# Kernel optimization log

Measured on AMD Instinct MI355X. Metric: run time of the kernel, lower is better.

The kernel has to match this reference:

```python
import jax, jax.numpy as jnp
import numpy as np

BLOCKS, LAYERS, KS = 4, 2, 2
DILATIONS = [2 ** i for _ in range(BLOCKS) for i in range(LAYERS)]  # [1,2]*4
B, C_IN, N, T = 16, 2, 2048, 12
RC, DC, SC, EC, OUT = 32, 32, 256, 512, 12
L = BLOCKS * LAYERS
BN_EPS = 1e-5


def setup_inputs() -> dict:
    key = jax.random.key(0)
    ks = jax.random.split(key, 24)
    # raw inputs
    x = jax.random.normal(ks[0], (B, C_IN, N, T), dtype=jnp.float32)
    # two fixed supports: row-normalized random adjacency (dense, as in GraphWaveNet transition matrices)
    A_raw = jax.random.uniform(ks[1], (2, N, N), dtype=jnp.float32)
    A = A_raw / jnp.sum(A_raw, axis=2, keepdims=True)
    nodevec1 = jax.random.normal(ks[2], (N, 10), dtype=jnp.float32)
    nodevec2 = jax.random.normal(ks[3], (10, N), dtype=jnp.float32)
    s = 0.1  # weight scale to keep activations in a sane range
    filter_w = jax.random.normal(ks[4], (L, DC, RC, KS), dtype=jnp.float32) * s
    filter_b = jax.random.normal(ks[5], (L, DC), dtype=jnp.float32) * s
    gate_w = jax.random.normal(ks[6], (L, DC, RC, KS), dtype=jnp.float32) * s
    gate_b = jax.random.normal(ks[7], (L, DC), dtype=jnp.float32) * s
    skip_w = jax.random.normal(ks[8], (L, SC, DC), dtype=jnp.float32) * s
    skip_b = jax.random.normal(ks[9], (L, SC), dtype=jnp.float32) * s
    gcn_w = jax.random.normal(ks[10], (L, RC, 7 * DC), dtype=jnp.float32) * s
    gcn_b = jax.random.normal(ks[11], (L, RC), dtype=jnp.float32) * s
    bn_gamma = 1.0 + 0.1 * jax.random.normal(ks[12], (L, RC), dtype=jnp.float32)
    bn_beta = 0.1 * jax.random.normal(ks[13], (L, RC), dtype=jnp.float32)
    bn_mean = 0.1 * jax.random.normal(ks[14], (L, RC), dtype=jnp.float32)
    bn_var = 1.0 + jax.random.uniform(ks[15], (L, RC), dtype=jnp.float32)
    start_w = jax.random.normal(ks[16], (RC, C_IN), dtype=jnp.float32) * s
    start_b = jax.random.normal(ks[17], (RC,), dtype=jnp.float32) * s
    end1_w = jax.random.normal(ks[18], (EC, SC), dtype=jnp.float32) * s
    end1_b = jax.random.normal(ks[19], (EC,), dtype=jnp.float32) * s
    end2_w = jax.random.normal(ks[20], (OUT, EC), dtype=jnp.float32) * s
    end2_b = jax.random.normal(ks[21], (OUT,), dtype=jnp.float32) * s
    return dict(x=x, A=A, nodevec1=nodevec1, nodevec2=nodevec2,
                filter_w=filter_w, filter_b=filter_b, gate_w=gate_w, gate_b=gate_b,
                skip_w=skip_w, skip_b=skip_b, gcn_w=gcn_w, gcn_b=gcn_b,
                bn_gamma=bn_gamma, bn_beta=bn_beta, bn_mean=bn_mean, bn_var=bn_var,
                start_w=start_w, start_b=start_b, end1_w=end1_w, end1_b=end1_b,
                end2_w=end2_w, end2_b=end2_b)


def _conv1x1(x, w, b):
    # x: [b,c,n,t], w: [o,c] -> [b,o,n,t]
    return jnp.einsum('oc,bcnt->bont', w, x) + b[None, :, None, None]


def _dilated_conv2(x, w, b, d):
    # kernel (1,2) with time dilation d; out length T-d (valid conv)
    xa, xb = x[..., :-d], x[..., d:]
    y = jnp.einsum('oc,bcnt->bont', w[:, :, 0], xa) + jnp.einsum('oc,bcnt->bont', w[:, :, 1], xb)
    return y + b[None, :, None, None]


def _fwd(x, A, nodevec1, nodevec2, filter_w, filter_b, gate_w, gate_b,
         skip_w, skip_b, gcn_w, gcn_b, bn_gamma, bn_beta, bn_mean, bn_var,
         start_w, start_b, end1_w, end1_b, end2_w, end2_b):
    # pad 1 step at the start of time; T becomes 13 == receptive_field
    x = jnp.pad(x, ((0, 0), (0, 0), (0, 0), (1, 0)))
    x = x[:, :2]
    x = _conv1x1(x, start_w, start_b)  # [B,RC,N,13]
    # adaptive adjacency
    adp = jax.nn.softmax(jax.nn.relu(nodevec1 @ nodevec2), axis=1)
    supports = [A[0], A[1], adp]
    skip = None
    for i, d in enumerate(DILATIONS):
        residual = x
        filt = jnp.tanh(_dilated_conv2(residual, filter_w[i], filter_b[i], d))
        gate = jax.nn.sigmoid(_dilated_conv2(residual, gate_w[i], gate_b[i], d))
        x = filt * gate  # [B,DC,N,T-d]
        s = _conv1x1(x, skip_w[i], skip_b[i])  # [B,SC,N,T']
        skip = s if skip is None else s + skip[..., -s.shape[3]:]
        # GCN: order-2 diffusion over 3 supports, concat, 1x1 mix (dropout is identity in eval)
        outs = [x]
        for a in supports:
            x1 = jnp.einsum('bcvt,vw->bcwt', x, a)
            x2 = jnp.einsum('bcvt,vw->bcwt', x1, a)
            outs.extend([x1, x2])
        h = jnp.concatenate(outs, axis=1)  # [B,7*DC,N,T']
        x = _conv1x1(h, gcn_w[i], gcn_b[i])
        x = x + residual[..., -x.shape[3]:]
        # BatchNorm2d in eval mode (running stats)
        inv = bn_gamma[i] / jnp.sqrt(bn_var[i] + BN_EPS)
        x = (x - bn_mean[i][None, :, None, None]) * inv[None, :, None, None] + bn_beta[i][None, :, None, None]
    x = jax.nn.relu(skip)
    x = jax.nn.relu(_conv1x1(x, end1_w, end1_b))
    x = _conv1x1(x, end2_w, end2_b)  # [B,OUT,N,1]
    return x


def reference(x, A, nodevec1, nodevec2, filter_w, filter_b, gate_w, gate_b,
              skip_w, skip_b, gcn_w, gcn_b, bn_gamma, bn_beta, bn_mean, bn_var,
              start_w, start_b, end1_w, end1_b, end2_w, end2_b):
    return _fwd(x, A, nodevec1, nodevec2, filter_w, filter_b, gate_w, gate_b,
                skip_w, skip_b, gcn_w, gcn_b, bn_gamma, bn_beta, bn_mean, bn_var,
                start_w, start_b, end1_w, end1_b, end2_w, end2_b)
```

## Files before the change

kernel.cpp:

```cpp
#include <hip/hip_runtime.h>
#include <math.h>


#define NNODE 2048
#define NLAYER 8
#define SSTR ((size_t)NNODE * NNODE)

typedef unsigned short u16;
typedef unsigned int u32;
typedef __attribute__((ext_vector_type(8))) short bf16x8;
typedef __attribute__((ext_vector_type(4))) float f32x4;

__device__ __forceinline__ u16 f2bf(float f) {
    unsigned u = __builtin_bit_cast(unsigned, f);
    u += 0x7fffu + ((u >> 16) & 1u);
    return (u16)(u >> 16);
}
__device__ __forceinline__ float bf2f(u16 h) {
    unsigned u = ((unsigned)h) << 16;
    return __builtin_bit_cast(float, u);
}
__device__ __forceinline__ float bflo(u32 p) { return __builtin_bit_cast(float, p << 16); }
__device__ __forceinline__ float bfhi(u32 p) { return __builtin_bit_cast(float, p & 0xffff0000u); }
__device__ __forceinline__ u32 pack2(float a, float b) {
    return (u32)f2bf(a) | ((u32)f2bf(b) << 16);
}

__device__ __forceinline__ void gld16(const void* g, void* l) {
    __builtin_amdgcn_global_load_lds(
        (const __attribute__((address_space(1))) unsigned int*)g,
        (__attribute__((address_space(3))) unsigned int*)l, 16, 0, 0);
}

__global__ __launch_bounds__(256) void k_adp_mm(const float* __restrict__ nv1,
                                                const float* __restrict__ nv2,
                                                float* __restrict__ P) {
    int v = blockIdx.y;
    int w = blockIdx.x * 256 + threadIdx.x;
    float acc = 0.f;
#pragma unroll
    for (int k = 0; k < 10; ++k) acc += nv1[v * 10 + k] * nv2[k * NNODE + w];
    P[(size_t)v * NNODE + w] = acc;
}

__global__ __launch_bounds__(256) void k_softmax(float* __restrict__ P) {
    int v = blockIdx.x, tid = threadIdx.x;
    float* row = P + (size_t)v * NNODE;
    float m = 0.f;
    for (int w = tid; w < NNODE; w += 256) m = fmaxf(m, fmaxf(row[w], 0.f));
#pragma unroll
    for (int off = 32; off > 0; off >>= 1) m = fmaxf(m, __shfl_down(m, off));
    __shared__ float redm[4];
    __shared__ float reds[4];
    int wave = tid >> 6, lane = tid & 63;
    if (lane == 0) redm[wave] = m;
    __syncthreads();
    m = fmaxf(fmaxf(redm[0], redm[1]), fmaxf(redm[2], redm[3]));
    float s = 0.f;
    for (int w = tid; w < NNODE; w += 256) s += expf(fmaxf(row[w], 0.f) - m);
#pragma unroll
    for (int off = 32; off > 0; off >>= 1) s += __shfl_down(s, off);
    if (lane == 0) reds[wave] = s;
    __syncthreads();
    s = reds[0] + reds[1] + reds[2] + reds[3];
    float inv = 1.f / s;
    for (int w = tid; w < NNODE; w += 256) row[w] = expf(fmaxf(row[w], 0.f) - m) * inv;
}

__global__ __launch_bounds__(256) void k_transp(const float* __restrict__ A,
                                                const float* __restrict__ adp,
                                                u16* __restrict__ ST,
                                                u16* __restrict__ Sbf) {
    __shared__ float tile[32][33];
    int s = blockIdx.z;
    const float* src = (s < 2) ? (A + (size_t)s * SSTR) : adp;
    int v0 = blockIdx.y * 32, w0 = blockIdx.x * 32;
    int tx = threadIdx.x & 31, ty = threadIdx.x >> 5;
    u16* dst2 = Sbf + (size_t)s * SSTR;
#pragma unroll
    for (int p = 0; p < 4; ++p) {
        float v = src[(size_t)(v0 + ty + p * 8) * NNODE + w0 + tx];
        tile[ty + p * 8][tx] = v;
        dst2[(size_t)(v0 + ty + p * 8) * NNODE + w0 + tx] = f2bf(v);
    }
    __syncthreads();
    u16* dst = ST + (size_t)(2 * s) * SSTR;
#pragma unroll
    for (int p = 0; p < 4; ++p)
        dst[(size_t)(w0 + ty + p * 8) * NNODE + v0 + tx] = f2bf(tile[tx][ty + p * 8]);
}

__global__ __launch_bounds__(256) void k_skprep(const float* __restrict__ skw,
                                                const float* __restrict__ skb,
                                                u16* __restrict__ skwB,
                                                float* __restrict__ skbsum) {
    int idx = blockIdx.x * 256 + threadIdx.x;
    int sc = idx >> 8, k = idx & 255, l = k >> 5, ci = k & 31;
    skwB[idx] = f2bf(skw[((size_t)l * 256 + sc) * 32 + ci]);
    if (blockIdx.x == 0) {
        float s = 0.f;
#pragma unroll
        for (int ll = 0; ll < 8; ++ll) s += skb[ll * 256 + threadIdx.x];
        skbsum[threadIdx.x] = s;
    }
}

__global__ __launch_bounds__(512, 2) void k_gemmS(const u16* __restrict__ ST,
                                                  const u16* __restrict__ Sbf) {
    __shared__ __align__(16) char ldsb[131072];
    const int tid = threadIdx.x;
    const int wave = tid >> 6, lane = tid & 63;
    const int m0 = blockIdx.y * 256;
    const int slice = blockIdx.x >> 3;
    const int n0 = (blockIdx.x & 7) * 256;
    const u16* AbG = ST + (size_t)(2 * slice) * SSTR + (size_t)m0 * 2048;
    const u16* BbG = Sbf + (size_t)slice * SSTR + (size_t)n0 * 2048;

    const int xorc = ((tid & 7) ^ ((tid >> 3) & 7)) << 3;
    const size_t aRow = (size_t)(tid >> 3) * 2048 + xorc;
    const int bRowLoc = ((tid >> 8) << 6) + (((tid >> 6) & 3) << 3) + ((tid >> 3) & 7);
    const size_t bRow = (size_t)bRowLoc * 2048 + xorc;
    const int aw = wave << 10;
    const int bw = ((wave >> 2) << 13) + ((wave & 3) << 10);

    const int fr = lane & 15;
    const int cl4 = lane >> 4;
    const int ch0 = (cl4 ^ (fr & 7)) << 4;
    const int ch1 = ch0 ^ 64;
    const int aRd = ((wave & 1) << 14) + fr * 128;
    const int bRd = ((wave >> 1) << 13) + fr * 128;
    const int wm = (wave & 1) << 7;
    const int wn = (wave >> 1) << 6;

    char* A0 = ldsb;
    char* A1 = ldsb + 32768;
    char* B0 = ldsb + 65536;
    char* B1 = ldsb + 98304;

    auto STA = [&](char* Abase, int k0, int q) {
        const size_t g = (size_t)(q << 6) * 2048 + aRow + k0;
        gld16(AbG + g, Abase + (q << 13) + aw);
        gld16(AbG + g + (size_t)128 * 2048, Abase + 16384 + (q << 13) + aw);
    };
    auto STB = [&](char* Bbase, int k0, int q) {
        const size_t g = (size_t)(q << 5) * 2048 + bRow + k0;
        gld16(BbG + g, Bbase + (q << 12) + bw);
        gld16(BbG + g + (size_t)128 * 2048, Bbase + 16384 + (q << 12) + bw);
    };

    f32x4 acc[8][4];
#pragma unroll
    for (int i = 0; i < 8; ++i)
#pragma unroll
        for (int j = 0; j < 4; ++j) acc[i][j] = (f32x4){0.f, 0.f, 0.f, 0.f};

    STA(A0, 0, 0); STA(A0, 0, 1); STB(B0, 0, 0); STB(B0, 0, 1);
    STA(A1, 64, 0); STB(B1, 64, 0); STB(B1, 64, 1);
    asm volatile("s_waitcnt vmcnt(6)" ::: "memory");
    asm volatile("s_barrier" ::: "memory");

    char *Ac = A0, *Ao = A1, *Bc = B0, *Bo = B1;
    bf16x8 af[4][2], bfl[2][2], bfh[2][2];

    for (int T = 0; T < 32; ++T) {
#pragma unroll
        for (int i = 0; i < 4; ++i) {
            af[i][0] = *(const bf16x8*)(Ac + aRd + (i << 11) + ch0);
            af[i][1] = *(const bf16x8*)(Ac + aRd + (i << 11) + ch1);
        }
#pragma unroll
        for (int j = 0; j < 2; ++j) {
            bfl[j][0] = *(const bf16x8*)(Bc + bRd + (j << 11) + ch0);
            bfl[j][1] = *(const bf16x8*)(Bc + bRd + (j << 11) + ch1);
        }
        if (T < 31) STA(Ao, (T + 1) * 64, 1);
        asm volatile("s_barrier" ::: "memory");
        asm volatile("s_waitcnt lgkmcnt(0)" ::: "memory");
        __builtin_amdgcn_sched_barrier(0);
        __builtin_amdgcn_s_setprio(1);
#pragma unroll
        for (int i = 0; i < 4; ++i)
#pragma unroll
            for (int j = 0; j < 2; ++j) {
                acc[i][j] = __builtin_amdgcn_mfma_f32_16x16x32_bf16(af[i][0], bfl[j][0], acc[i][j], 0, 0, 0);
                acc[i][j] = __builtin_amdgcn_mfma_f32_16x16x32_bf16(af[i][1], bfl[j][1], acc[i][j], 0, 0, 0);
            }
        __builtin_amdgcn_s_setprio(0);
#pragma unroll
        for (int j = 0; j < 2; ++j) {
            bfh[j][0] = *(const bf16x8*)(Bc + bRd + 4096 + (j << 11) + ch0);
            bfh[j][1] = *(const bf16x8*)(Bc + bRd + 4096 + (j << 11) + ch1);
        }
        asm volatile("s_barrier" ::: "memory");
        asm volatile("s_waitcnt lgkmcnt(0)" ::: "memory");
        __builtin_amdgcn_sched_barrier(0);
        __builtin_amdgcn_s_setprio(1);
#pragma unroll
        for (int i = 0; i < 4; ++i)
#pragma unroll
            for (int j = 0; j < 2; ++j) {
                acc[i][2 + j] = __builtin_amdgcn_mfma_f32_16x16x32_bf16(af[i][0], bfh[j][0], acc[i][2 + j], 0, 0, 0);
                acc[i][2 + j] = __builtin_amdgcn_mfma_f32_16x16x32_bf16(af[i][1], bfh[j][1], acc[i][2 + j], 0, 0, 0);
            }
        __builtin_amdgcn_s_setprio(0);
#pragma unroll
        for (int i = 0; i < 4; ++i) {
            af[i][0] = *(const bf16x8*)(Ac + aRd + 8192 + (i << 11) + ch0);
            af[i][1] = *(const bf16x8*)(Ac + aRd + 8192 + (i << 11) + ch1);
        }
        if (T < 30) { STA(Ac, (T + 2) * 64, 0); STB(Bc, (T + 2) * 64, 0); }
        asm volatile("s_barrier" ::: "memory");
        asm volatile("s_waitcnt lgkmcnt(0)" ::: "memory");
        __builtin_amdgcn_sched_barrier(0);
        __builtin_amdgcn_s_setprio(1);
#pragma unroll
        for (int i = 0; i < 4; ++i)
#pragma unroll
            for (int j = 0; j < 2; ++j) {
                acc[4 + i][2 + j] = __builtin_amdgcn_mfma_f32_16x16x32_bf16(af[i][0], bfh[j][0], acc[4 + i][2 + j], 0, 0, 0);
                acc[4 + i][2 + j] = __builtin_amdgcn_mfma_f32_16x16x32_bf16(af[i][1], bfh[j][1], acc[4 + i][2 + j], 0, 0, 0);
            }
        __builtin_amdgcn_s_setprio(0);
        if (T < 30) STB(Bc, (T + 2) * 64, 1);
        asm volatile("s_barrier" ::: "memory");
        __builtin_amdgcn_sched_barrier(0);
        __builtin_amdgcn_s_setprio(1);
#pragma unroll
        for (int i = 0; i < 4; ++i)
#pragma unroll
            for (int j = 0; j < 2; ++j) {
                acc[4 + i][j] = __builtin_amdgcn_mfma_f32_16x16x32_bf16(af[i][0], bfl[j][0], acc[4 + i][j], 0, 0, 0);
                acc[4 + i][j] = __builtin_amdgcn_mfma_f32_16x16x32_bf16(af[i][1], bfl[j][1], acc[4 + i][j], 0, 0, 0);
            }
        __builtin_amdgcn_s_setprio(0);
        if (T < 30) {
            asm volatile("s_waitcnt vmcnt(6)" ::: "memory");
        } else if (T == 30) {
            asm volatile("s_waitcnt vmcnt(0)" ::: "memory");
        }
        asm volatile("s_barrier" ::: "memory");
        char* t;
        t = Ac; Ac = Ao; Ao = t;
        t = Bc; Bc = Bo; Bo = t;
    }

    u16* Cb = (u16*)ST + (size_t)(2 * slice + 1) * SSTR + (size_t)(m0 + wm) * 2048 + n0 + wn;
    const int orow = cl4 * 4;
#pragma unroll
    for (int i = 0; i < 8; ++i)
#pragma unroll
        for (int j = 0; j < 4; ++j)
#pragma unroll
            for (int r = 0; r < 4; ++r)
                Cb[(size_t)(i * 16 + orow + r) * 2048 + j * 16 + fr] = f2bf(acc[i][j][r]);
}

__global__ __launch_bounds__(512, 2) void k_gemmZ(const u16* __restrict__ Xg,
                                                  const u16* __restrict__ ST,
                                                  u16* __restrict__ Z, int pass) {
    __shared__ __align__(16) char ldsb[131072];
    const int tid = threadIdx.x;
    const int wave = tid >> 6, lane = tid & 63;
    const int m0 = blockIdx.y * 256;
    const int slice = pass * 3 + (blockIdx.x >> 3);
    const int n0 = (blockIdx.x & 7) * 256;
    const u16* AbG = Xg + (size_t)m0 * 2048;
    const u16* BbG = ST + (size_t)slice * SSTR + (size_t)n0 * 2048;

    const int xorc = ((tid & 7) ^ ((tid >> 3) & 7)) << 3;
    const size_t aRow = (size_t)(tid >> 3) * 2048 + xorc;
    const int bRowLoc = ((tid >> 8) << 6) + (((tid >> 6) & 3) << 3) + ((tid >> 3) & 7);
    const size_t bRow = (size_t)bRowLoc * 2048 + xorc;
    const int aw = wave << 10;
    const int bw = ((wave >> 2) << 13) + ((wave & 3) << 10);

    const int fr = lane & 15;
    const int cl4 = lane >> 4;
    const int ch0 = (cl4 ^ (fr & 7)) << 4;
    const int ch1 = ch0 ^ 64;
    const int aRd = ((wave & 1) << 14) + fr * 128;
    const int bRd = ((wave >> 1) << 13) + fr * 128;
    const int wm = (wave & 1) << 7;
    const int wn = (wave >> 1) << 6;

    char* A0 = ldsb;
    char* A1 = ldsb + 32768;
    char* B0 = ldsb + 65536;
    char* B1 = ldsb + 98304;

    auto STA = [&](char* Abase, int k0, int q) {
        const size_t g = (size_t)(q << 6) * 2048 + aRow + k0;
        gld16(AbG + g, Abase + (q << 13) + aw);
        gld16(AbG + g + (size_t)128 * 2048, Abase + 16384 + (q << 13) + aw);
    };
    auto STB = [&](char* Bbase, int k0, int q) {
        const size_t g = (size_t)(q << 5) * 2048 + bRow + k0;
        gld16(BbG + g, Bbase + (q << 12) + bw);
        gld16(BbG + g + (size_t)128 * 2048, Bbase + 16384 + (q << 12) + bw);
    };

    f32x4 acc[8][4];
#pragma unroll
    for (int i = 0; i < 8; ++i)
#pragma unroll
        for (int j = 0; j < 4; ++j) acc[i][j] = (f32x4){0.f, 0.f, 0.f, 0.f};

    STA(A0, 0, 0); STA(A0, 0, 1); STB(B0, 0, 0); STB(B0, 0, 1);
    STA(A1, 64, 0); STB(B1, 64, 0); STB(B1, 64, 1);
    asm volatile("s_waitcnt vmcnt(6)" ::: "memory");
    asm volatile("s_barrier" ::: "memory");

    char *Ac = A0, *Ao = A1, *Bc = B0, *Bo = B1;
    bf16x8 af[4][2], bfl[2][2], bfh[2][2];

    for (int T = 0; T < 32; ++T) {
#pragma unroll
        for (int i = 0; i < 4; ++i) {
            af[i][0] = *(const bf16x8*)(Ac + aRd + (i << 11) + ch0);
            af[i][1] = *(const bf16x8*)(Ac + aRd + (i << 11) + ch1);
        }
#pragma unroll
        for (int j = 0; j < 2; ++j) {
            bfl[j][0] = *(const bf16x8*)(Bc + bRd + (j << 11) + ch0);
            bfl[j][1] = *(const bf16x8*)(Bc + bRd + (j << 11) + ch1);
        }
        if (T < 31) STA(Ao, (T + 1) * 64, 1);
        asm volatile("s_barrier" ::: "memory");
        asm volatile("s_waitcnt lgkmcnt(0)" ::: "memory");
        __builtin_amdgcn_sched_barrier(0);
        __builtin_amdgcn_s_setprio(1);
#pragma unroll
        for (int i = 0; i < 4; ++i)
#pragma unroll
            for (int j = 0; j < 2; ++j) {
                acc[i][j] = __builtin_amdgcn_mfma_f32_16x16x32_bf16(af[i][0], bfl[j][0], acc[i][j], 0, 0, 0);
                acc[i][j] = __builtin_amdgcn_mfma_f32_16x16x32_bf16(af[i][1], bfl[j][1], acc[i][j], 0, 0, 0);
            }
        __builtin_amdgcn_s_setprio(0);
#pragma unroll
        for (int j = 0; j < 2; ++j) {
            bfh[j][0] = *(const bf16x8*)(Bc + bRd + 4096 + (j << 11) + ch0);
            bfh[j][1] = *(const bf16x8*)(Bc + bRd + 4096 + (j << 11) + ch1);
        }
        asm volatile("s_barrier" ::: "memory");
        asm volatile("s_waitcnt lgkmcnt(0)" ::: "memory");
        __builtin_amdgcn_sched_barrier(0);
        __builtin_amdgcn_s_setprio(1);
#pragma unroll
        for (int i = 0; i < 4; ++i)
#pragma unroll
            for (int j = 0; j < 2; ++j) {
                acc[i][2 + j] = __builtin_amdgcn_mfma_f32_16x16x32_bf16(af[i][0], bfh[j][0], acc[i][2 + j], 0, 0, 0);
                acc[i][2 + j] = __builtin_amdgcn_mfma_f32_16x16x32_bf16(af[i][1], bfh[j][1], acc[i][2 + j], 0, 0, 0);
            }
        __builtin_amdgcn_s_setprio(0);
#pragma unroll
        for (int i = 0; i < 4; ++i) {
            af[i][0] = *(const bf16x8*)(Ac + aRd + 8192 + (i << 11) + ch0);
            af[i][1] = *(const bf16x8*)(Ac + aRd + 8192 + (i << 11) + ch1);
        }
        if (T < 30) { STA(Ac, (T + 2) * 64, 0); STB(Bc, (T + 2) * 64, 0); }
        asm volatile("s_barrier" ::: "memory");
        asm volatile("s_waitcnt lgkmcnt(0)" ::: "memory");
        __builtin_amdgcn_sched_barrier(0);
        __builtin_amdgcn_s_setprio(1);
#pragma unroll
        for (int i = 0; i < 4; ++i)
#pragma unroll
            for (int j = 0; j < 2; ++j) {
                acc[4 + i][2 + j] = __builtin_amdgcn_mfma_f32_16x16x32_bf16(af[i][0], bfh[j][0], acc[4 + i][2 + j], 0, 0, 0);
                acc[4 + i][2 + j] = __builtin_amdgcn_mfma_f32_16x16x32_bf16(af[i][1], bfh[j][1], acc[4 + i][2 + j], 0, 0, 0);
            }
        __builtin_amdgcn_s_setprio(0);
        if (T < 30) STB(Bc, (T + 2) * 64, 1);
        asm volatile("s_barrier" ::: "memory");
        __builtin_amdgcn_sched_barrier(0);
        __builtin_amdgcn_s_setprio(1);
#pragma unroll
        for (int i = 0; i < 4; ++i)
#pragma unroll
            for (int j = 0; j < 2; ++j) {
                acc[4 + i][j] = __builtin_amdgcn_mfma_f32_16x16x32_bf16(af[i][0], bfl[j][0], acc[4 + i][j], 0, 0, 0);
                acc[4 + i][j] = __builtin_amdgcn_mfma_f32_16x16x32_bf16(af[i][1], bfl[j][1], acc[4 + i][j], 0, 0, 0);
            }
        __builtin_amdgcn_s_setprio(0);
        if (T < 30) {
            asm volatile("s_waitcnt vmcnt(6)" ::: "memory");
        } else if (T == 30) {
            asm volatile("s_waitcnt vmcnt(0)" ::: "memory");
        }
        asm volatile("s_barrier" ::: "memory");
        char* t;
        t = Ac; Ac = Ao; Ao = t;
        t = Bc; Bc = Bo; Bo = t;
    }

    const int col0 = (blockIdx.x >> 3) * 2048 + (blockIdx.x & 7) * 256;
    u16* Cb = Z + (size_t)(m0 + wm) * 6144 + col0 + wn;
    const int orow = cl4 * 4;
#pragma unroll
    for (int i = 0; i < 8; ++i)
#pragma unroll
        for (int j = 0; j < 4; ++j)
#pragma unroll
            for (int r = 0; r < 4; ++r)
                Cb[(size_t)(i * 16 + orow + r) * 6144 + j * 16 + fr] = f2bf(acc[i][j][r]);
}

__global__ __launch_bounds__(256) void k_gemmZ128(const u16* __restrict__ Xg,
                                                  const u16* __restrict__ ST,
                                                  u16* __restrict__ Z, int pass) {
    __shared__ u16 Asl[2][128 * 32];
    __shared__ u16 Bsl[2][128 * 32];
    const int tid = threadIdx.x;
    const int wave = tid >> 6, lane = tid & 63;
    const int m0 = blockIdx.y * 128;
    const int slice = pass * 3 + (blockIdx.x >> 4);
    const int nIn = (blockIdx.x & 15) * 128;
    const u16* Ab = Xg + (size_t)m0 * 2048;
    const u16* Bb = ST + (size_t)slice * SSTR + (size_t)nIn * NNODE;
    const int tr = tid >> 2;
    const int tc = (tid & 3) * 8;
    char* AslB0 = (char*)Asl[0] + wave * 1024;
    char* AslB1 = (char*)Asl[1] + wave * 1024;
    char* BslB0 = (char*)Bsl[0] + wave * 1024;
    char* BslB1 = (char*)Bsl[1] + wave * 1024;
    const int wm = (wave & 1) * 64, wn = (wave >> 1) * 64;
    const int fr = lane & 15;
    const int fk = (lane >> 4) * 8;
    f32x4 acc[4][4];
#pragma unroll
    for (int i = 0; i < 4; ++i)
#pragma unroll
        for (int j = 0; j < 4; ++j) acc[i][j] = (f32x4){0.f, 0.f, 0.f, 0.f};

    for (int k0 = 0; k0 < 2048; k0 += 64) {
        gld16(Ab + (size_t)tr * 2048 + k0 + tc, AslB0);
        gld16(Ab + (size_t)(tr + 64) * 2048 + k0 + tc, AslB0 + 4096);
        gld16(Ab + (size_t)tr * 2048 + k0 + 32 + tc, AslB1);
        gld16(Ab + (size_t)(tr + 64) * 2048 + k0 + 32 + tc, AslB1 + 4096);
        gld16(Bb + (size_t)tr * NNODE + k0 + tc, BslB0);
        gld16(Bb + (size_t)(tr + 64) * NNODE + k0 + tc, BslB0 + 4096);
        gld16(Bb + (size_t)tr * NNODE + k0 + 32 + tc, BslB1);
        gld16(Bb + (size_t)(tr + 64) * NNODE + k0 + 32 + tc, BslB1 + 4096);
        __syncthreads();
#pragma unroll
        for (int h = 0; h < 2; ++h) {
            bf16x8 af[4], bf[4];
#pragma unroll
            for (int i = 0; i < 4; ++i)
                af[i] = *(const bf16x8*)&Asl[h][(wm + i * 16 + fr) * 32 + fk];
#pragma unroll
            for (int j = 0; j < 4; ++j)
                bf[j] = *(const bf16x8*)&Bsl[h][(wn + j * 16 + fr) * 32 + fk];
#pragma unroll
            for (int i = 0; i < 4; ++i)
#pragma unroll
                for (int j = 0; j < 4; ++j)
                    acc[i][j] = __builtin_amdgcn_mfma_f32_16x16x32_bf16(af[i], bf[j], acc[i][j], 0, 0, 0);
        }
        __syncthreads();
    }
    u16* Cb = Z + (size_t)(m0 + wm) * 6144 + blockIdx.x * 128 + wn;
    const int orow = (lane >> 4) * 4;
#pragma unroll
    for (int i = 0; i < 4; ++i)
#pragma unroll
        for (int j = 0; j < 4; ++j)
#pragma unroll
            for (int r = 0; r < 4; ++r)
                Cb[(size_t)(i * 16 + orow + r) * 6144 + j * 16 + fr] = f2bf(acc[i][j][r]);
}

__global__ __launch_bounds__(256) void k_start(const float* __restrict__ xin,
                                               const float* __restrict__ sw,
                                               const float* __restrict__ sb,
                                               u16* __restrict__ out, int b0) {
    int n = blockIdx.x * 256 + threadIdx.x;
    int t = blockIdx.y;
    int bl = blockIdx.z;
    int b = b0 + bl;
    float x0 = 0.f, x1 = 0.f;
    if (t > 0) {
        x0 = xin[((size_t)(b * 2 + 0) * NNODE + n) * 12 + (t - 1)];
        x1 = xin[((size_t)(b * 2 + 1) * NNODE + n) * 12 + (t - 1)];
    }
#pragma unroll
    for (int co = 0; co < 32; ++co) {
        float v = sw[co * 2 + 0] * x0 + sw[co * 2 + 1] * x1 + sb[co];
        out[((size_t)(bl * 32 + co) * 13 + t) * NNODE + n] = f2bf(v);
    }
}

__global__ __launch_bounds__(256) void k_gate(const u16* __restrict__ cur,
                                              u16* __restrict__ xg,
                                              u16* __restrict__ nxt,
                                              int T, int Tn, int d,
                                              const float* __restrict__ fw,
                                              const float* __restrict__ fb,
                                              const float* __restrict__ gw,
                                              const float* __restrict__ gb,
                                              const float* __restrict__ gcwl,
                                              const float* __restrict__ gcbl,
                                              u16* __restrict__ xl,
                                              int layer, int donxt) {
    __shared__ float4 wp[1024];
    __shared__ float w0[32][33];
    int tid = threadIdx.x;
#pragma unroll
    for (int u = 0; u < 4; ++u) {
        int idx = tid + u * 256;
        int ci = idx >> 5, co = idx & 31;
        wp[idx] = make_float4(fw[co * 64 + ci * 2], fw[co * 64 + ci * 2 + 1],
                              gw[co * 64 + ci * 2], gw[co * 64 + ci * 2 + 1]);
        w0[ci][co] = gcwl[co * 224 + ci];
    }
    __syncthreads();
    int n = blockIdx.x * 512 + tid * 2;
    int t = blockIdx.y;
    int bl = blockIdx.z;
    float f0[32], f1[32], g0[32], g1[32];
#pragma unroll
    for (int co = 0; co < 32; ++co) { f0[co] = 0.f; f1[co] = 0.f; g0[co] = 0.f; g1[co] = 0.f; }
    for (int ci = 0; ci < 32; ++ci) {
        size_t ba = ((size_t)(bl * 32 + ci) * T + t) * NNODE + n;
        size_t bb = ((size_t)(bl * 32 + ci) * T + t + d) * NNODE + n;
        u32 ua = *(const u32*)&cur[ba];
        u32 ub = *(const u32*)&cur[bb];
        float xa0 = bflo(ua), xa1 = bfhi(ua);
        float xb0 = bflo(ub), xb1 = bfhi(ub);
#pragma unroll
        for (int co = 0; co < 32; ++co) {
            float4 w = wp[ci * 32 + co];
            f0[co] += w.x * xa0 + w.y * xb0;
            f1[co] += w.x * xa1 + w.y * xb1;
            g0[co] += w.z * xa0 + w.w * xb0;
            g1[co] += w.z * xa1 + w.w * xb1;
        }
    }
#pragma unroll
    for (int co = 0; co < 32; ++co) {
        float fbv = fb[co], gbv = gb[co];
        float a0 = tanhf(f0[co] + fbv) * (1.f / (1.f + expf(-(g0[co] + gbv))));
        float a1 = tanhf(f1[co] + fbv) * (1.f / (1.f + expf(-(g1[co] + gbv))));
        f0[co] = a0; f1[co] = a1;
        size_t o = ((size_t)(bl * 32 + co) * Tn + t) * NNODE + n;
        *(u32*)&xg[o] = pack2(a0, a1);
    }
    if (t == Tn - 1) {
        size_t o2 = ((size_t)(bl * 2048 + n)) * 256 + layer * 32;
#pragma unroll
        for (int co = 0; co < 32; ++co) {
            xl[o2 + co] = f2bf(f0[co]);
            xl[o2 + 256 + co] = f2bf(f1[co]);
        }
    }
    if (donxt) {
#pragma unroll
        for (int cop = 0; cop < 32; ++cop) {
            float s0 = gcbl[cop], s1 = s0;
#pragma unroll
            for (int ci = 0; ci < 32; ++ci) {
                float wv = w0[ci][cop];
                s0 += wv * f0[ci];
                s1 += wv * f1[ci];
            }
            size_t o = ((size_t)(bl * 32 + cop) * Tn + t) * NNODE + n;
            *(u32*)&nxt[o] = pack2(s0, s1);
        }
    }
}

__global__ __launch_bounds__(256) void k_accum(const u16* __restrict__ Z,
                                               int cbase,
                                               const float* __restrict__ gcnw,
                                               u16* __restrict__ outp,
                                               const u16* __restrict__ resid,
                                               int Tn, int d, int finalf,
                                               const float* __restrict__ bng,
                                               const float* __restrict__ bnb,
                                               const float* __restrict__ bnm,
                                               const float* __restrict__ bnv) {
    __shared__ float wl[3][32][32];
    int tid = threadIdx.x;
    for (int u = tid; u < 3072; u += 256) {
        int g = u >> 10, ci = (u >> 5) & 31, co = u & 31;
        wl[g][ci][co] = gcnw[co * 224 + cbase + g * 32 + ci];
    }
    __syncthreads();
    int n = blockIdx.x * 512 + tid * 2;
    int t = blockIdx.y, bl = blockIdx.z;
    float a0[32], a1[32];
#pragma unroll
    for (int co = 0; co < 32; ++co) { a0[co] = 0.f; a1[co] = 0.f; }
    for (int ci = 0; ci < 32; ++ci) {
        size_t m = (size_t)(bl * 32 + ci) * Tn + t;
#pragma unroll
        for (int g = 0; g < 3; ++g) {
            u32 zz = *(const u32*)&Z[m * 6144 + g * 2048 + n];
            float v0 = bflo(zz), v1 = bfhi(zz);
#pragma unroll
            for (int cq = 0; cq < 8; ++cq) {
                float4 w = *(const float4*)&wl[g][ci][cq * 4];
                a0[cq * 4 + 0] += w.x * v0; a1[cq * 4 + 0] += w.x * v1;
                a0[cq * 4 + 1] += w.y * v0; a1[cq * 4 + 1] += w.y * v1;
                a0[cq * 4 + 2] += w.z * v0; a1[cq * 4 + 2] += w.z * v1;
                a0[cq * 4 + 3] += w.w * v0; a1[cq * 4 + 3] += w.w * v1;
            }
        }
    }
#pragma unroll
    for (int co = 0; co < 32; ++co) {
        size_t o = ((size_t)(bl * 32 + co) * Tn + t) * NNODE + n;
        u32 oo = *(const u32*)&outp[o];
        float v0 = bflo(oo) + a0[co];
        float v1 = bfhi(oo) + a1[co];
        if (finalf) {
            size_t ro = ((size_t)(bl * 32 + co) * (Tn + d) + t + d) * NNODE + n;
            u32 rr = *(const u32*)&resid[ro];
            v0 += bflo(rr); v1 += bfhi(rr);
            float inv = bng[co] * rsqrtf(bnv[co] + 1e-5f);
            float mu = bnm[co], be = bnb[co];
            v0 = (v0 - mu) * inv + be;
            v1 = (v1 - mu) * inv + be;
        }
        *(u32*)&outp[o] = pack2(v0, v1);
    }
}

__global__ __launch_bounds__(256) void k_accum2(const u16* __restrict__ Z0,
                                                const u16* __restrict__ Z1,
                                                const float* __restrict__ gcnw,
                                                u16* __restrict__ outp,
                                                const u16* __restrict__ resid,
                                                int Tn, int d,
                                                const float* __restrict__ bng,
                                                const float* __restrict__ bnb,
                                                const float* __restrict__ bnm,
                                                const float* __restrict__ bnv) {
    __shared__ float wl[6][32][32];
    int tid = threadIdx.x;
    for (int u = tid; u < 6144; u += 256) {
        int pg = u >> 10, ci = (u >> 5) & 31, co = u & 31;
        int cbase = (pg < 3) ? (32 + pg * 32) : (128 + (pg - 3) * 32);
        wl[pg][ci][co] = gcnw[co * 224 + cbase + ci];
    }
    __syncthreads();
    int n = blockIdx.x * 512 + tid * 2;
    int t = blockIdx.y, bl = blockIdx.z;
    float a0[32], a1[32];
#pragma unroll
    for (int co = 0; co < 32; ++co) { a0[co] = 0.f; a1[co] = 0.f; }
    for (int ci = 0; ci < 32; ++ci) {
        size_t m = (size_t)(bl * 32 + ci) * Tn + t;
#pragma unroll
        for (int pg = 0; pg < 6; ++pg) {
            const u16* Zs = (pg < 3) ? Z0 : Z1;
            int g = (pg < 3) ? pg : pg - 3;
            u32 zz = *(const u32*)&Zs[m * 6144 + g * 2048 + n];
            float v0 = bflo(zz), v1 = bfhi(zz);
#pragma unroll
            for (int cq = 0; cq < 8; ++cq) {
                float4 w = *(const float4*)&wl[pg][ci][cq * 4];
                a0[cq * 4 + 0] += w.x * v0; a1[cq * 4 + 0] += w.x * v1;
                a0[cq * 4 + 1] += w.y * v0; a1[cq * 4 + 1] += w.y * v1;
                a0[cq * 4 + 2] += w.z * v0; a1[cq * 4 + 2] += w.z * v1;
                a0[cq * 4 + 3] += w.w * v0; a1[cq * 4 + 3] += w.w * v1;
            }
        }
    }
#pragma unroll
    for (int co = 0; co < 32; ++co) {
        size_t o = ((size_t)(bl * 32 + co) * Tn + t) * NNODE + n;
        u32 oo = *(const u32*)&outp[o];
        float v0 = bflo(oo) + a0[co];
        float v1 = bfhi(oo) + a1[co];
        size_t ro = ((size_t)(bl * 32 + co) * (Tn + d) + t + d) * NNODE + n;
        u32 rr = *(const u32*)&resid[ro];
        v0 += bflo(rr); v1 += bfhi(rr);
        float inv = bng[co] * rsqrtf(bnv[co] + 1e-5f);
        float mu = bnm[co], be = bnb[co];
        v0 = (v0 - mu) * inv + be;
        v1 = (v1 - mu) * inv + be;
        *(u32*)&outp[o] = pack2(v0, v1);
    }
}

__global__ __launch_bounds__(256) void k_cast(const float* __restrict__ src,
                                              u16* __restrict__ dst) {
    int i = blockIdx.x * 256 + threadIdx.x;
    dst[i] = f2bf(src[i]);
}

__global__ __launch_bounds__(256) void k_skipg(const u16* __restrict__ xl,
                                               const u16* __restrict__ skwB,
                                               const float* __restrict__ skbsum,
                                               u16* __restrict__ skipT) {
    __shared__ u16 Asl[128 * 32];
    __shared__ u16 Bsl[128 * 32];
    const int tid = threadIdx.x;
    const int wave = tid >> 6, lane = tid & 63;
    const int m0 = blockIdx.y * 128;
    const int n0 = blockIdx.x * 128;
    const int tr = tid >> 2;
    const int tc = (tid & 3) * 8;
    char* AslB = (char*)Asl + wave * 1024;
    char* BslB = (char*)Bsl + wave * 1024;
    const int wm = (wave & 1) * 64, wn = (wave >> 1) * 64;
    const int fr = lane & 15;
    const int fk = (lane >> 4) * 8;
    const u16* Ab = xl + (size_t)m0 * 256;
    const u16* Bb = skwB + (size_t)n0 * 256;
    f32x4 acc[4][4];
#pragma unroll
    for (int i = 0; i < 4; ++i)
#pragma unroll
        for (int j = 0; j < 4; ++j) acc[i][j] = (f32x4){0.f, 0.f, 0.f, 0.f};
    for (int k0 = 0; k0 < 256; k0 += 32) {
        gld16(Ab + (size_t)tr * 256 + k0 + tc, AslB);
        gld16(Ab + (size_t)(tr + 64) * 256 + k0 + tc, AslB + 4096);
        gld16(Bb + (size_t)tr * 256 + k0 + tc, BslB);
        gld16(Bb + (size_t)(tr + 64) * 256 + k0 + tc, BslB + 4096);
        __syncthreads();
        bf16x8 af[4], bf[4];
#pragma unroll
        for (int i = 0; i < 4; ++i)
            af[i] = *(const bf16x8*)&Asl[(wm + i * 16 + fr) * 32 + fk];
#pragma unroll
        for (int j = 0; j < 4; ++j)
            bf[j] = *(const bf16x8*)&Bsl[(wn + j * 16 + fr) * 32 + fk];
#pragma unroll
        for (int i = 0; i < 4; ++i)
#pragma unroll
            for (int j = 0; j < 4; ++j)
                acc[i][j] = __builtin_amdgcn_mfma_f32_16x16x32_bf16(af[i], bf[j], acc[i][j], 0, 0, 0);
        __syncthreads();
    }
    const int orow = (lane >> 4) * 4;
#pragma unroll
    for (int i = 0; i < 4; ++i)
#pragma unroll
        for (int r = 0; r < 4; ++r) {
            int m = m0 + wm + i * 16 + orow + r;
            size_t ob = (size_t)m * 256 + n0 + wn;
#pragma unroll
            for (int j = 0; j < 4; ++j) {
                int col = n0 + wn + j * 16 + fr;
                skipT[ob + j * 16 + fr] = f2bf(fmaxf(acc[i][j][r] + skbsum[col], 0.f));
            }
        }
}

__global__ __launch_bounds__(256) void k_end1m(const u16* __restrict__ E1,
                                               const u16* __restrict__ skT,
                                               const float* __restrict__ bias,
                                               u16* __restrict__ h) {
    __shared__ u16 Asl[128 * 32];
    __shared__ u16 Bsl[128 * 32];
    const int tid = threadIdx.x;
    const int wave = tid >> 6, lane = tid & 63;
    const int b = blockIdx.z;
    const int m0 = blockIdx.y * 128;
    const int n0 = blockIdx.x * 128;
    const int tr = tid >> 2;
    const int tc = (tid & 3) * 8;
    char* AslB = (char*)Asl + wave * 1024;
    char* BslB = (char*)Bsl + wave * 1024;
    const int wm = (wave & 1) * 64, wn = (wave >> 1) * 64;
    const int fr = lane & 15;
    const int fk = (lane >> 4) * 8;
    const u16* Ab = E1 + (size_t)m0 * 256;
    const u16* Bb = skT + ((size_t)b * NNODE + n0) * 256;
    f32x4 acc[4][4];
#pragma unroll
    for (int i = 0; i < 4; ++i)
#pragma unroll
        for (int j = 0; j < 4; ++j) acc[i][j] = (f32x4){0.f, 0.f, 0.f, 0.f};
    for (int k0 = 0; k0 < 256; k0 += 32) {
        gld16(Ab + (size_t)tr * 256 + k0 + tc, AslB);
        gld16(Ab + (size_t)(tr + 64) * 256 + k0 + tc, AslB + 4096);
        gld16(Bb + (size_t)tr * 256 + k0 + tc, BslB);
        gld16(Bb + (size_t)(tr + 64) * 256 + k0 + tc, BslB + 4096);
        __syncthreads();
        bf16x8 af[4], bf[4];
#pragma unroll
        for (int i = 0; i < 4; ++i)
            af[i] = *(const bf16x8*)&Asl[(wm + i * 16 + fr) * 32 + fk];
#pragma unroll
        for (int j = 0; j < 4; ++j)
            bf[j] = *(const bf16x8*)&Bsl[(wn + j * 16 + fr) * 32 + fk];
#pragma unroll
        for (int i = 0; i < 4; ++i)
#pragma unroll
            for (int j = 0; j < 4; ++j)
                acc[i][j] = __builtin_amdgcn_mfma_f32_16x16x32_bf16(af[i], bf[j], acc[i][j], 0, 0, 0);
        __syncthreads();
    }
    const int orow = (lane >> 4) * 4;
#pragma unroll
    for (int i = 0; i < 4; ++i)
#pragma unroll
        for (int r = 0; r < 4; ++r) {
            int m = m0 + wm + i * 16 + orow + r;
            float bs = bias[m];
            size_t ob = ((size_t)b * 512 + m) * NNODE + n0 + wn;
#pragma unroll
            for (int j = 0; j < 4; ++j)
                h[ob + j * 16 + fr] = f2bf(fmaxf(acc[i][j][r] + bs, 0.f));
        }
}

__global__ __launch_bounds__(256) void k_end2(const u16* __restrict__ h,
                                              const float* __restrict__ w,
                                              const float* __restrict__ bias,
                                              float* __restrict__ out) {
    __shared__ float wl[12][512];
    int tid = threadIdx.x;
    for (int u = tid; u < 6144; u += 256) wl[u >> 9][u & 511] = w[u];
    __syncthreads();
    int n = blockIdx.x * 256 + tid;
    int b = blockIdx.y;
    float acc[12];
#pragma unroll
    for (int o = 0; o < 12; ++o) acc[o] = 0.f;
#pragma unroll 4
    for (int e = 0; e < 512; ++e) {
        float v = bf2f(h[((size_t)(b * 512) + e) * NNODE + n]);
#pragma unroll
        for (int o = 0; o < 12; ++o) acc[o] += wl[o][e] * v;
    }
#pragma unroll
    for (int o = 0; o < 12; ++o)
        out[((size_t)(b * 12) + o) * NNODE + n] = acc[o] + bias[o];
}

extern "C" void kernel_launch(void* const* d_in, const int* in_sizes, int n_in,
                              void* d_out, int out_size, void* d_ws, size_t ws_size,
                              hipStream_t stream) {
    const float* x_in = (const float*)d_in[0];
    const float* A    = (const float*)d_in[1];
    const float* nv1  = (const float*)d_in[2];
    const float* nv2  = (const float*)d_in[3];
    const float* fw   = (const float*)d_in[4];
    const float* fb   = (const float*)d_in[5];
    const float* gw   = (const float*)d_in[6];
    const float* gb   = (const float*)d_in[7];
    const float* skw  = (const float*)d_in[8];
    const float* skb  = (const float*)d_in[9];
    const float* gcw  = (const float*)d_in[10];
    const float* gcb  = (const float*)d_in[11];
    const float* bng  = (const float*)d_in[12];
    const float* bnb  = (const float*)d_in[13];
    const float* bnm  = (const float*)d_in[14];
    const float* bnv  = (const float*)d_in[15];
    const float* stw  = (const float*)d_in[16];
    const float* stb  = (const float*)d_in[17];
    const float* e1w  = (const float*)d_in[18];
    const float* e1b  = (const float*)d_in[19];
    const float* e2w  = (const float*)d_in[20];
    const float* e2b  = (const float*)d_in[21];
    (void)in_sizes; (void)n_in; (void)out_size;

    const int BL = (ws_size >= 239075328UL) ? 16 : 8;
    const int nch = 16 / BL;
    const size_t bufsz = (size_t)BL * 1703936UL;

    char* base = (char*)d_ws;
    u16*   ST     = (u16*)base;
    u16*   xlast  = (u16*)(base + 50331648UL);
    u16*   skwB   = (u16*)(base + 67108864UL);
    float* skbsum = (float*)(base + 67239936UL);
    u16*   bufA = (u16*)(base + 83886080UL);
    u16*   bufB = (u16*)(base + 83886080UL + bufsz);
    u16*   xg   = (u16*)(base + 83886080UL + 2 * bufsz);
    u16*   Z    = (u16*)(base + 83886080UL + 2 * bufsz + (size_t)BL * 1572864UL);
    float* adp  = (float*)Z;
    u16*   Sbf  = (u16*)bufA;
    u16*   h     = (u16*)(base + 83886080UL);
    u16*   skipT = (u16*)(base + 83886080UL + 33554432UL);
    u16*   E1bf  = (u16*)ST;

    k_adp_mm<<<dim3(8, 2048), 256, 0, stream>>>(nv1, nv2, adp);
    k_skprep<<<256, 256, 0, stream>>>(skw, skb, skwB, skbsum);
    k_softmax<<<2048, 256, 0, stream>>>(adp);
    k_transp<<<dim3(64, 64, 3), 256, 0, stream>>>(A, adp, ST, Sbf);
    k_gemmS<<<dim3(24, 8), 512, 0, stream>>>(ST, Sbf);

    static const int DIL[NLAYER] = {1, 2, 1, 2, 1, 2, 1, 2};
    for (int ch = 0; ch < nch; ++ch) {
        int b0 = ch * BL;
        k_start<<<dim3(8, 13, BL), 256, 0, stream>>>(x_in, stw, stb, bufA, b0);
        u16* cur = bufA;
        u16* nxt = bufB;
        int T = 13;
        for (int i = 0; i < NLAYER; ++i) {
            int d = DIL[i], Tn = T - d;
            int last = (i == NLAYER - 1);
            k_gate<<<dim3(4, Tn, BL), 256, 0, stream>>>(cur, xg, nxt, T, Tn, d,
                fw + i * 2048, fb + i * 32, gw + i * 2048, gb + i * 32,
                gcw + i * 32 * 224, gcb + i * 32,
                xlast + (size_t)b0 * 2048 * 256, i, last ? 0 : 1);
            if (last) break;
            const float* gcwi = gcw + i * 32 * 224;
            const size_t Msz = (size_t)BL * 32 * Tn * 6144;
            const bool canMerge =
                (BL == 16) && (Tn <= 6 || (Tn == 7 && ws_size >= 251658240UL));
            if (Tn == 6 || Tn == 3) {
                if (canMerge) {
                    k_gemmZ128<<<dim3(48, BL * Tn / 4), 256, 0, stream>>>(xg, ST, Z, 0);
                    k_gemmZ128<<<dim3(48, BL * Tn / 4), 256, 0, stream>>>(xg, ST, Z + Msz, 1);
                    k_accum2<<<dim3(4, Tn, BL), 256, 0, stream>>>(
                        Z, Z + Msz, gcwi, nxt, cur, Tn, d,
                        bng + i * 32, bnb + i * 32, bnm + i * 32, bnv + i * 32);
                } else {
                    for (int p = 0; p < 2; ++p) {
                        k_gemmZ128<<<dim3(48, BL * Tn / 4), 256, 0, stream>>>(xg, ST, Z, p);
                        k_accum<<<dim3(4, Tn, BL), 256, 0, stream>>>(
                            Z, 32 + 96 * p, gcwi, nxt, cur, Tn, d, p,
                            bng + i * 32, bnb + i * 32, bnm + i * 32, bnv + i * 32);
                    }
                }
            } else if (canMerge) {
                k_gemmZ<<<dim3(24, BL * 32 * Tn / 256), 512, 0, stream>>>(xg, ST, Z, 0);
                k_gemmZ<<<dim3(24, BL * 32 * Tn / 256), 512, 0, stream>>>(xg, ST, Z + Msz, 1);
                k_accum2<<<dim3(4, Tn, BL), 256, 0, stream>>>(
                    Z, Z + Msz, gcwi, nxt, cur, Tn, d,
                    bng + i * 32, bnb + i * 32, bnm + i * 32, bnv + i * 32);
            } else {
                for (int p = 0; p < 2; ++p) {
                    k_gemmZ<<<dim3(24, BL * 32 * Tn / 256), 512, 0, stream>>>(xg, ST, Z, p);
                    k_accum<<<dim3(4, Tn, BL), 256, 0, stream>>>(
                        Z, 32 + 96 * p, gcwi, nxt, cur, Tn, d, p,
                        bng + i * 32, bnb + i * 32, bnm + i * 32, bnv + i * 32);
                }
            }
            u16* tmp = cur; cur = nxt; nxt = tmp;
            T = Tn;
        }
    }
    k_cast<<<512, 256, 0, stream>>>(e1w, E1bf);
    k_skipg<<<dim3(2, 256), 256, 0, stream>>>(xlast, skwB, skbsum, skipT);
    k_end1m<<<dim3(16, 4, 16), 256, 0, stream>>>(E1bf, skipT, e1b, h);
    k_end2<<<dim3(8, 16), 256, 0, stream>>>(h, e2w, e2b, (float*)d_out);
}
```

Baseline: 2.917 ms.

## Fuse adaptive adjacency matmul with softmax and rebalance the Tn=12 GEMM grid

Merges the nodevec product and the row softmax into one kernel that keeps each row in registers, removing a full write and re-read of the 2048x2048 float matrix. For the Tn=12 layer it replaces two equal GEMM launches with a 32-row-block launch, where the extra blocks compute part of pass 1 into a spare Zx buffer, and a 16-row-block launch for the rest. A new accumulate kernel reads from either buffer depending on the row. It also sends Tn=7 to the 128-tile GEMM path. The aim is better wave quantization across the GPU's compute units, at the cost of more complex buffer bookkeeping and a dependence on a larger workspace.

```diff
diff --git a/kernel.cpp b/kernel.cpp
--- a/kernel.cpp
+++ b/kernel.cpp
@@ -32,22 +32,25 @@
         (__attribute__((address_space(3))) unsigned int*)l, 16, 0, 0);
 }
 
-__global__ __launch_bounds__(256) void k_adp_mm(const float* __restrict__ nv1,
-                                                const float* __restrict__ nv2,
-                                                float* __restrict__ P) {
-    int v = blockIdx.y;
-    int w = blockIdx.x * 256 + threadIdx.x;
-    float acc = 0.f;
-#pragma unroll
-    for (int k = 0; k < 10; ++k) acc += nv1[v * 10 + k] * nv2[k * NNODE + w];
-    P[(size_t)v * NNODE + w] = acc;
-}
-
-__global__ __launch_bounds__(256) void k_softmax(float* __restrict__ P) {
+__global__ __launch_bounds__(256) void k_adpsm(const float* __restrict__ nv1,
+                                               const float* __restrict__ nv2,
+                                               float* __restrict__ P) {
     int v = blockIdx.x, tid = threadIdx.x;
-    float* row = P + (size_t)v * NNODE;
+    float a[10];
+#pragma unroll
+    for (int k = 0; k < 10; ++k) a[k] = nv1[v * 10 + k];
+    float val[8];
     float m = 0.f;
-    for (int w = tid; w < NNODE; w += 256) m = fmaxf(m, fmaxf(row[w], 0.f));
+#pragma unroll
+    for (int u = 0; u < 8; ++u) {
+        int w = tid + u * 256;
+        float acc = 0.f;
+#pragma unroll
+        for (int k = 0; k < 10; ++k) acc += a[k] * nv2[k * NNODE + w];
+        acc = fmaxf(acc, 0.f);
+        val[u] = acc;
+        m = fmaxf(m, acc);
+    }
 #pragma unroll
     for (int off = 32; off > 0; off >>= 1) m = fmaxf(m, __shfl_down(m, off));
     __shared__ float redm[4];
@@ -57,14 +60,17 @@
     __syncthreads();
     m = fmaxf(fmaxf(redm[0], redm[1]), fmaxf(redm[2], redm[3]));
     float s = 0.f;
-    for (int w = tid; w < NNODE; w += 256) s += expf(fmaxf(row[w], 0.f) - m);
+#pragma unroll
+    for (int u = 0; u < 8; ++u) { val[u] = expf(val[u] - m); s += val[u]; }
 #pragma unroll
     for (int off = 32; off > 0; off >>= 1) s += __shfl_down(s, off);
     if (lane == 0) reds[wave] = s;
     __syncthreads();
     s = reds[0] + reds[1] + reds[2] + reds[3];
     float inv = 1.f / s;
-    for (int w = tid; w < NNODE; w += 256) row[w] = expf(fmaxf(row[w], 0.f) - m) * inv;
+#pragma unroll
+    for (int u = 0; u < 8; ++u)
+        P[(size_t)v * NNODE + tid + u * 256] = val[u] * inv;
 }
 
 __global__ __launch_bounds__(256) void k_transp(const float* __restrict__ A,
@@ -257,12 +263,18 @@
 
 __global__ __launch_bounds__(512, 2) void k_gemmZ(const u16* __restrict__ Xg,
                                                   const u16* __restrict__ ST,
-                                                  u16* __restrict__ Z, int pass) {
+                                                  u16* __restrict__ Z, int pass,
+                                                  int mbMain, int mOff,
+                                                  u16* __restrict__ Zx) {
     __shared__ __align__(16) char ldsb[131072];
     const int tid = threadIdx.x;
     const int wave = tid >> 6, lane = tid & 63;
-    const int m0 = blockIdx.y * 256;
-    const int slice = pass * 3 + (blockIdx.x >> 3);
+    int byv = blockIdx.y;
+    int p = pass;
+    u16* Zo = Z;
+    if (byv >= mbMain) { byv -= mbMain; p = 1; Zo = Zx; }
+    const int m0 = (byv + mOff) * 256;
+    const int slice = p * 3 + (blockIdx.x >> 3);
     const int n0 = (blockIdx.x & 7) * 256;
     const u16* AbG = Xg + (size_t)m0 * 2048;
     const u16* BbG = ST + (size_t)slice * SSTR + (size_t)n0 * 2048;
@@ -396,7 +408,7 @@
     }
 
     const int col0 = (blockIdx.x >> 3) * 2048 + (blockIdx.x & 7) * 256;
-    u16* Cb = Z + (size_t)(m0 + wm) * 6144 + col0 + wn;
+    u16* Cb = Zo + (size_t)(m0 + wm) * 6144 + col0 + wn;
     const int orow = cl4 * 4;
 #pragma unroll
     for (int i = 0; i < 8; ++i)
@@ -624,6 +636,63 @@
             v0 = (v0 - mu) * inv + be;
             v1 = (v1 - mu) * inv + be;
         }
+        *(u32*)&outp[o] = pack2(v0, v1);
+    }
+}
+
+__global__ __launch_bounds__(256) void k_accumX(const u16* __restrict__ Z,
+                                                const u16* __restrict__ Zx,
+                                                int splitRow,
+                                                const float* __restrict__ gcnw,
+                                                u16* __restrict__ outp,
+                                                const u16* __restrict__ resid,
+                                                int Tn, int d,
+                                                const float* __restrict__ bng,
+                                                const float* __restrict__ bnb,
+                                                const float* __restrict__ bnm,
+                                                const float* __restrict__ bnv) {
+    __shared__ float wl[3][32][32];
+    int tid = threadIdx.x;
+    for (int u = tid; u < 3072; u += 256) {
+        int g = u >> 10, ci = (u >> 5) & 31, co = u & 31;
+        wl[g][ci][co] = gcnw[co * 224 + 128 + g * 32 + ci];
+    }
+    __syncthreads();
+    int n = blockIdx.x * 512 + tid * 2;
+    int t = blockIdx.y, bl = blockIdx.z;
+    float a0[32], a1[32];
+#pragma unroll
+    for (int co = 0; co < 32; ++co) { a0[co] = 0.f; a1[co] = 0.f; }
+    for (int ci = 0; ci < 32; ++ci) {
+        size_t m = (size_t)(bl * 32 + ci) * Tn + t;
+        const u16* Zs = (m < (size_t)splitRow) ? Zx : Z;
+#pragma unroll
+        for (int g = 0; g < 3; ++g) {
+            u32 zz = *(const u32*)&Zs[m * 6144 + g * 2048 + n];
+            float v0 = bflo(zz), v1 = bfhi(zz);
+#pragma unroll
+            for (int cq = 0; cq < 8; ++cq) {
+                float4 w = *(const float4*)&wl[g][ci][cq * 4];
+                a0[cq * 4 + 0] += w.x * v0; a1[cq * 4 + 0] += w.x * v1;
+                a0[cq * 4 + 1] += w.y * v0; a1[cq * 4 + 1] += w.y * v1;
+                a0[cq * 4 + 2] += w.z * v0; a1[cq * 4 + 2] += w.z * v1;
+                a0[cq * 4 + 3] += w.w * v0; a1[cq * 4 + 3] += w.w * v1;
+            }
+        }
+    }
+#pragma unroll
+    for (int co = 0; co < 32; ++co) {
+        size_t o = ((size_t)(bl * 32 + co) * Tn + t) * NNODE + n;
+        u32 oo = *(const u32*)&outp[o];
+        float v0 = bflo(oo) + a0[co];
+        float v1 = bfhi(oo) + a1[co];
+        size_t ro = ((size_t)(bl * 32 + co) * (Tn + d) + t + d) * NNODE + n;
+        u32 rr = *(const u32*)&resid[ro];
+        v0 += bflo(rr); v1 += bfhi(rr);
+        float inv = bng[co] * rsqrtf(bnv[co] + 1e-5f);
+        float mu = bnm[co], be = bnb[co];
+        v0 = (v0 - mu) * inv + be;
+        v1 = (v1 - mu) * inv + be;
         *(u32*)&outp[o] = pack2(v0, v1);
     }
 }
@@ -874,15 +943,15 @@
     u16*   bufB = (u16*)(base + 83886080UL + bufsz);
     u16*   xg   = (u16*)(base + 83886080UL + 2 * bufsz);
     u16*   Z    = (u16*)(base + 83886080UL + 2 * bufsz + (size_t)BL * 1572864UL);
+    u16*   Zx   = (u16*)(base + 239075328UL);
     float* adp  = (float*)Z;
     u16*   Sbf  = (u16*)bufA;
     u16*   h     = (u16*)(base + 83886080UL);
     u16*   skipT = (u16*)(base + 83886080UL + 33554432UL);
     u16*   E1bf  = (u16*)ST;
 
-    k_adp_mm<<<dim3(8, 2048), 256, 0, stream>>>(nv1, nv2, adp);
+    k_adpsm<<<2048, 256, 0, stream>>>(nv1, nv2, adp);
     k_skprep<<<256, 256, 0, stream>>>(skw, skb, skwB, skbsum);
-    k_softmax<<<2048, 256, 0, stream>>>(adp);
     k_transp<<<dim3(64, 64, 3), 256, 0, stream>>>(A, adp, ST, Sbf);
     k_gemmS<<<dim3(24, 8), 512, 0, stream>>>(ST, Sbf);
 
@@ -905,7 +974,7 @@
             const size_t Msz = (size_t)BL * 32 * Tn * 6144;
             const bool canMerge =
                 (BL == 16) && (Tn <= 6 || (Tn == 7 && ws_size >= 251658240UL));
-            if (Tn == 6 || Tn == 3) {
+            if (Tn == 6 || Tn == 3 || Tn == 7) {
                 if (canMerge) {
                     k_gemmZ128<<<dim3(48, BL * Tn / 4), 256, 0, stream>>>(xg, ST, Z, 0);
                     k_gemmZ128<<<dim3(48, BL * Tn / 4), 256, 0, stream>>>(xg, ST, Z + Msz, 1);
@@ -920,15 +989,27 @@
                             bng + i * 32, bnb + i * 32, bnm + i * 32, bnv + i * 32);
                     }
                 }
+            } else if (Tn == 12 && BL == 16 && ws_size >= 264241152UL) {
+                k_gemmZ<<<dim3(24, 32), 512, 0, stream>>>(xg, ST, Z, 0, 24, 0, Zx);
+                k_accum<<<dim3(4, Tn, BL), 256, 0, stream>>>(
+                    Z, 32, gcwi, nxt, cur, Tn, d, 0,
+                    bng + i * 32, bnb + i * 32, bnm + i * 32, bnv + i * 32);
+                k_gemmZ<<<dim3(24, 16), 512, 0, stream>>>(xg, ST, Z, 1, 1 << 20, 8, (u16*)0);
+                k_accumX<<<dim3(4, Tn, BL), 256, 0, stream>>>(
+                    Z, Zx, 2048, gcwi, nxt, cur, Tn, d,
+                    bng + i * 32, bnb + i * 32, bnm + i * 32, bnv + i * 32);
             } else if (canMerge) {
-                k_gemmZ<<<dim3(24, BL * 32 * Tn / 256), 512, 0, stream>>>(xg, ST, Z, 0);
-                k_gemmZ<<<dim3(24, BL * 32 * Tn / 256), 512, 0, stream>>>(xg, ST, Z + Msz, 1);
+                k_gemmZ<<<dim3(24, BL * 32 * Tn / 256), 512, 0, stream>>>(
+                    xg, ST, Z, 0, 1 << 20, 0, (u16*)0);
+                k_gemmZ<<<dim3(24, BL * 32 * Tn / 256), 512, 0, stream>>>(
+                    xg, ST, Z + Msz, 1, 1 << 20, 0, (u16*)0);
                 k_accum2<<<dim3(4, Tn, BL), 256, 0, stream>>>(
                     Z, Z + Msz, gcwi, nxt, cur, Tn, d,
                     bng + i * 32, bnb + i * 32, bnm + i * 32, bnv + i * 32);
             } else {
                 for (int p = 0; p < 2; ++p) {
-                    k_gemmZ<<<dim3(24, BL * 32 * Tn / 256), 512, 0, stream>>>(xg, ST, Z, p);
+                    k_gemmZ<<<dim3(24, BL * 32 * Tn / 256), 512, 0, stream>>>(
+                        xg, ST, Z, p, 1 << 20, 0, (u16*)0);
                     k_accum<<<dim3(4, Tn, BL), 256, 0, stream>>>(
                         Z, 32 + 96 * p, gcwi, nxt, cur, Tn, d, p,
                         bng + i * 32, bnb + i * 32, bnm + i * 32, bnv + i * 32);
```

Measured after the change: 2.804 ms. 3.9% less time.
